# Performance work log

Hardware: AMD Instinct MI355X
Metric: run time of the kernel (lower is better)

The kernel has to match this reference:

```python
import jax, jax.numpy as jnp
import numpy as np

DIM = 1024
HEADS = 16
DIM_HEAD = 64


def setup_inputs() -> dict:
    key = jax.random.key(0)
    ks = jax.random.split(key, 6)
    b, n = 2, 2048
    x = jax.random.normal(ks[0], (b, n, DIM), dtype=jnp.float32)
    gamma = jnp.ones((DIM,), dtype=jnp.float32)
    w_qkv = jax.random.normal(ks[1], (DIM, 3 * HEADS * DIM_HEAD), dtype=jnp.float32) * (DIM ** -0.5)
    w_gates = jax.random.normal(ks[2], (DIM, HEADS), dtype=jnp.float32) * (DIM ** -0.5)
    b_gates = jnp.zeros((HEADS,), dtype=jnp.float32)
    w_out = jax.random.normal(ks[3], (HEADS * DIM_HEAD, DIM), dtype=jnp.float32) * ((HEADS * DIM_HEAD) ** -0.5)
    freqs = jax.random.uniform(ks[4], (DIM_HEAD // 2,), dtype=jnp.float32)
    return {"x": x, "gamma": gamma, "w_qkv": w_qkv, "w_gates": w_gates,
            "b_gates": b_gates, "w_out": w_out, "freqs": freqs}


def _rotate_half(t):
    # interleaved pairs: (x1, x2) -> (-x2, x1)
    tp = t.reshape(t.shape[:-1] + (t.shape[-1] // 2, 2))
    x1, x2 = tp[..., 0], tp[..., 1]
    return jnp.stack((-x2, x1), axis=-1).reshape(t.shape)


def reference(x, gamma, w_qkv, w_gates, b_gates, w_out, freqs):
    b, n, d = x.shape
    # RMSNorm variant: divide by L2 norm, scale by gamma * sqrt(dim)
    xn = x / jnp.linalg.norm(x, axis=-1, keepdims=True)
    xn = xn * gamma * (d ** 0.5)
    # QKV projection: (b, n, 3*H*D) -> q,k,v each (b, h, n, dh)
    qkv = xn @ w_qkv
    qkv = qkv.reshape(b, n, 3, HEADS, DIM_HEAD).transpose(2, 0, 3, 1, 4)
    q, k, v = qkv[0], qkv[1], qkv[2]
    # Inline RoPE (interleaved): freqs (n, dh)
    pos = jnp.arange(n, dtype=freqs.dtype)
    f = jnp.repeat(pos[:, None] * freqs[None, :], 2, axis=-1)  # (n, dh)
    cos_f, sin_f = jnp.cos(f), jnp.sin(f)
    q = q * cos_f + _rotate_half(q) * sin_f
    k = k * cos_f + _rotate_half(k) * sin_f
    # SDPA
    scale = DIM_HEAD ** -0.5
    scores = jnp.einsum('bhqd,bhkd->bhqk', q, k) * scale
    attn = jax.nn.softmax(scores, axis=-1)
    out = jnp.einsum('bhqk,bhkd->bhqd', attn, v)  # (b, h, n, dh)
    # per-head sigmoid gate from normalized input
    gates = xn @ w_gates + b_gates  # (b, n, h)
    out = out * jax.nn.sigmoid(gates.transpose(0, 2, 1))[..., None]
    # merge heads and output projection
    out = out.transpose(0, 2, 1, 3).reshape(b, n, HEADS * DIM_HEAD)
    return out @ w_out
```

## Files before the change

### kernel.cpp

```cpp
#include <hip/hip_runtime.h>

typedef __bf16 bf16_t;
typedef __bf16 bf16x8 __attribute__((ext_vector_type(8)));
typedef __bf16 bf16x4 __attribute__((ext_vector_type(4)));
typedef float f32x4 __attribute__((ext_vector_type(4)));

#define B_  2
#define N_  2048
#define D_  1024
#define H_  16
#define DH_ 64

#define GLL16(g, l) __builtin_amdgcn_global_load_lds( \
    (const __attribute__((address_space(1))) void*)(g), \
    (__attribute__((address_space(3))) void*)(l), 16, 0, 0)

__global__ __launch_bounds__(256) void k_rmsnorm_gates(const float* __restrict__ x,
    const float* __restrict__ gamma, const float* __restrict__ wg,
    const float* __restrict__ bg, bf16_t* __restrict__ xn, float* __restrict__ gsig) {
  int row = blockIdx.x;
  const float4* xr = (const float4*)(x + (size_t)row * D_);
  int tid = threadIdx.x;
  float4 v = xr[tid];
  float ss = v.x*v.x + v.y*v.y + v.z*v.z + v.w*v.w;
  #pragma unroll
  for (int off = 32; off > 0; off >>= 1) ss += __shfl_down(ss, off);
  __shared__ float red4[4];
  if ((tid & 63) == 0) red4[tid >> 6] = ss;
  __syncthreads();
  float scale = 32.0f * rsqrtf(red4[0] + red4[1] + red4[2] + red4[3]);
  float4 g = ((const float4*)gamma)[tid];
  bf16x4 o;
  o[0] = (bf16_t)(v.x * scale * g.x);
  o[1] = (bf16_t)(v.y * scale * g.y);
  o[2] = (bf16_t)(v.z * scale * g.z);
  o[3] = (bf16_t)(v.w * scale * g.w);
  *(bf16x4*)(xn + (size_t)row * D_ + tid * 4) = o;
  float xv[4] = {(float)o[0], (float)o[1], (float)o[2], (float)o[3]};
  float part[16];
  #pragma unroll
  for (int h = 0; h < 16; ++h) part[h] = 0.f;
  #pragma unroll
  for (int j = 0; j < 4; ++j) {
    const float4* wr = (const float4*)&wg[(size_t)(tid * 4 + j) * 16];
    #pragma unroll
    for (int q = 0; q < 4; ++q) {
      float4 w4 = wr[q];
      part[q * 4 + 0] += xv[j] * w4.x;
      part[q * 4 + 1] += xv[j] * w4.y;
      part[q * 4 + 2] += xv[j] * w4.z;
      part[q * 4 + 3] += xv[j] * w4.w;
    }
  }
  __shared__ float red[256][17];
  #pragma unroll
  for (int h = 0; h < 16; ++h) red[tid][h] = part[h];
  __syncthreads();
  int h = tid & 15, grp = tid >> 4;
  float s = 0.f;
  #pragma unroll
  for (int k = 0; k < 16; ++k) s += red[grp * 16 + k][h];
  __syncthreads();
  red[grp][h] = s;
  __syncthreads();
  if (tid < 16) {
    float acc = bg[tid];
    #pragma unroll
    for (int k = 0; k < 16; ++k) acc += red[k][tid];
    gsig[(size_t)row * 16 + tid] = 1.0f / (1.0f + __expf(-acc));
  }
}

__global__ __launch_bounds__(256) void k_transpose_cvt(const float* __restrict__ W,
    bf16_t* __restrict__ Wt, int R, int C) {
  __shared__ float tile[32][33];
  int c0 = blockIdx.x * 32, r0 = blockIdx.y * 32;
  int tx = threadIdx.x & 31, ty = threadIdx.x >> 5;
  #pragma unroll
  for (int i = 0; i < 4; ++i) {
    int r = ty + i * 8;
    tile[r][tx] = W[(size_t)(r0 + r) * C + c0 + tx];
  }
  __syncthreads();
  #pragma unroll
  for (int i = 0; i < 4; ++i) {
    int rr = ty + i * 8;
    Wt[(size_t)(c0 + rr) * R + r0 + tx] = (bf16_t)tile[tx][rr];
  }
}

template<bool OUT_BF16>
__global__ __launch_bounds__(256) void k_gemm_bt(const bf16_t* __restrict__ A,
    const bf16_t* __restrict__ Bt, void* __restrict__ Cp, int M, int N, int K) {
  constexpr int BK = 32;
  __shared__ __align__(16) bf16_t As[128 * BK];
  __shared__ __align__(16) bf16_t Bs[128 * BK];
  int tid = threadIdx.x, wave = tid >> 6, lane = tid & 63;
  int l16 = lane & 15, quad = lane >> 4;
  int bm = blockIdx.x * 128, bn = blockIdx.y * 128;
  int wm = (wave >> 1) * 64, wn = (wave & 1) * 64;
  int srow = wave * 32 + (lane >> 2);
  int scol = (lane & 3) * 8;
  const bf16_t* gA0 = &A [(size_t)(bm + srow)      * K + scol];
  const bf16_t* gA1 = &A [(size_t)(bm + srow + 16) * K + scol];
  const bf16_t* gB0 = &Bt[(size_t)(bn + srow)      * K + scol];
  const bf16_t* gB1 = &Bt[(size_t)(bn + srow + 16) * K + scol];
  bf16_t* lA0 = &As[(wave * 32)      * BK];
  bf16_t* lA1 = &As[(wave * 32 + 16) * BK];
  bf16_t* lB0 = &Bs[(wave * 32)      * BK];
  bf16_t* lB1 = &Bs[(wave * 32 + 16) * BK];
  f32x4 acc[4][4] = {};
  for (int k0 = 0; k0 < K; k0 += BK) {
    GLL16(gA0 + k0, lA0);
    GLL16(gA1 + k0, lA1);
    GLL16(gB0 + k0, lB0);
    GLL16(gB1 + k0, lB1);
    __syncthreads();
    bf16x8 af[4], bfr[4];
    #pragma unroll
    for (int t = 0; t < 4; ++t) {
      af[t]  = *(const bf16x8*)&As[(wm + t * 16 + l16) * BK + quad * 8];
      bfr[t] = *(const bf16x8*)&Bs[(wn + t * 16 + l16) * BK + quad * 8];
    }
    #pragma unroll
    for (int mt = 0; mt < 4; ++mt)
      #pragma unroll
      for (int nt = 0; nt < 4; ++nt)
        acc[mt][nt] = __builtin_amdgcn_mfma_f32_16x16x32_bf16(af[mt], bfr[nt], acc[mt][nt], 0, 0, 0);
    __syncthreads();
  }
  #pragma unroll
  for (int mt = 0; mt < 4; ++mt)
    #pragma unroll
    for (int nt = 0; nt < 4; ++nt)
      #pragma unroll
      for (int r = 0; r < 4; ++r) {
        int row = bm + wm + mt * 16 + quad * 4 + r;
        int col = bn + wn + nt * 16 + l16;
        float v = acc[mt][nt][r];
        if (OUT_BF16) ((bf16_t*)Cp)[(size_t)row * N + col] = (bf16_t)v;
        else          ((float*)Cp)[(size_t)row * N + col] = v;
      }
}

__global__ __launch_bounds__(256) void k_rope(const bf16_t* __restrict__ qkvb,
    const float* __restrict__ freqs, bf16_t* __restrict__ Qb, bf16_t* __restrict__ Kb) {
  int row = blockIdx.x, b = row >> 11, n = row & 2047;
  __shared__ float cs[32], sn[32];
  int tid = threadIdx.x;
  if (tid < 32) { float f = (float)n * freqs[tid]; cs[tid] = cosf(f); sn[tid] = sinf(f); }
  __syncthreads();
  const bf16_t* src = qkvb + (size_t)row * 3072;
  #pragma unroll
  for (int it = 0; it < 2; ++it) {
    int p = tid + 256 * it;
    int h = p >> 5, j = p & 31;
    size_t dst = ((size_t)(b * H_ + h) * N_ + n) * DH_ + 2 * j;
    float c = cs[j], s = sn[j];
    {
      float v0 = (float)src[h * 64 + 2 * j], v1 = (float)src[h * 64 + 2 * j + 1];
      union { bf16_t q[2]; unsigned u; } pk;
      pk.q[0] = (bf16_t)((v0 * c - v1 * s) * 0.125f);
      pk.q[1] = (bf16_t)((v1 * c + v0 * s) * 0.125f);
      *(unsigned*)&Qb[dst] = pk.u;
    }
    {
      float v0 = (float)src[1024 + h * 64 + 2 * j], v1 = (float)src[1024 + h * 64 + 2 * j + 1];
      union { bf16_t q[2]; unsigned u; } pk;
      pk.q[0] = (bf16_t)(v0 * c - v1 * s);
      pk.q[1] = (bf16_t)(v1 * c + v0 * s);
      *(unsigned*)&Kb[dst] = pk.u;
    }
  }
}

__global__ __launch_bounds__(256) void k_vtrans(const bf16_t* __restrict__ qkvb,
    bf16_t* __restrict__ Vb) {
  __shared__ bf16_t Vs[64][72];
  int bh = blockIdx.x, nt = blockIdx.y;
  int b = bh >> 4, h = bh & 15;
  int n0 = nt * 64;
  int tid = threadIdx.x;
  #pragma unroll
  for (int it = 0; it < 2; ++it) {
    int chunk = tid + 256 * it;
    int nl = chunk >> 3, c = (chunk & 7) * 8;
    *(bf16x8*)&Vs[nl][c] =
        *(const bf16x8*)&qkvb[(size_t)(b * N_ + n0 + nl) * 3072 + 2048 + h * 64 + c];
  }
  __syncthreads();
  #pragma unroll
  for (int it = 0; it < 2; ++it) {
    int chunk = tid + 256 * it;
    int d = chunk >> 3, nc = (chunk & 7) * 8;
    bf16x8 o;
    #pragma unroll
    for (int jj = 0; jj < 8; ++jj) o[jj] = Vs[nc + jj][d];
    *(bf16x8*)&Vb[((size_t)bh * DH_ + d) * N_ + n0 + nc] = o;
  }
}

__global__ __launch_bounds__(256) void k_flash(const bf16_t* __restrict__ Qb,
    const bf16_t* __restrict__ Kb, const bf16_t* __restrict__ Vb,
    const float* __restrict__ gsig, bf16_t* __restrict__ Ao) {
  __shared__ __align__(16) bf16_t Ks[2][64 * 72];
  __shared__ __align__(16) bf16_t Vt[2][64 * 72];
  __shared__ __align__(16) bf16_t Ps[4][32 * 72];
  int bh = blockIdx.y, b = bh >> 4, h = bh & 15;
  int tid = threadIdx.x, wave = tid >> 6, lane = tid & 63;
  int l16 = lane & 15, quad = lane >> 4;
  int qw = blockIdx.x * 128 + wave * 32;
  const bf16_t* Qh = Qb + (size_t)bh * N_ * DH_;
  const bf16_t* Kh = Kb + (size_t)bh * N_ * DH_;
  const bf16_t* Vh = Vb + (size_t)bh * DH_ * N_;
  bf16_t* Pw = Ps[wave];
  bf16x8 qf[2][2];
  #pragma unroll
  for (int qt = 0; qt < 2; ++qt)
    #pragma unroll
    for (int hf = 0; hf < 2; ++hf)
      qf[qt][hf] = *(const bf16x8*)&Qh[(size_t)(qw + qt * 16 + l16) * DH_ + hf * 32 + quad * 8];
  f32x4 accO[2][4] = {};
  float lsum[2] = {0.f, 0.f};
  int sk = tid >> 3;
  int sc = (tid & 7) * 8;
  bf16x8 rk0 = *(const bf16x8*)&Kh[(size_t)sk * DH_ + sc];
  bf16x8 rk1 = *(const bf16x8*)&Kh[(size_t)(sk + 32) * DH_ + sc];
  bf16x8 rv0 = *(const bf16x8*)&Vh[(size_t)sk * N_ + sc];
  bf16x8 rv1 = *(const bf16x8*)&Vh[(size_t)(sk + 32) * N_ + sc];
  *(bf16x8*)&Ks[0][sk * 72 + sc]        = rk0;
  *(bf16x8*)&Ks[0][(sk + 32) * 72 + sc] = rk1;
  *(bf16x8*)&Vt[0][sk * 72 + sc]        = rv0;
  *(bf16x8*)&Vt[0][(sk + 32) * 72 + sc] = rv1;
  __syncthreads();
  for (int k0 = 0; k0 < N_; k0 += 64) {
    int cur = (k0 >> 6) & 1;
    const bf16_t* Kc = Ks[cur];
    const bf16_t* Vc = Vt[cur];
    int kn = k0 + 64;
    if (kn < N_) {
      rk0 = *(const bf16x8*)&Kh[(size_t)(kn + sk) * DH_ + sc];
      rk1 = *(const bf16x8*)&Kh[(size_t)(kn + sk + 32) * DH_ + sc];
      rv0 = *(const bf16x8*)&Vh[(size_t)sk * N_ + kn + sc];
      rv1 = *(const bf16x8*)&Vh[(size_t)(sk + 32) * N_ + kn + sc];
    }
    f32x4 st[4][2];
    __builtin_amdgcn_s_setprio(1);
    #pragma unroll
    for (int kt = 0; kt < 4; ++kt) {
      bf16x8 kf0 = *(const bf16x8*)&Kc[(kt * 16 + l16) * 72 + quad * 8];
      bf16x8 kf1 = *(const bf16x8*)&Kc[(kt * 16 + l16) * 72 + 32 + quad * 8];
      #pragma unroll
      for (int qt = 0; qt < 2; ++qt) {
        f32x4 z = {};
        z = __builtin_amdgcn_mfma_f32_16x16x32_bf16(kf0, qf[qt][0], z, 0, 0, 0);
        z = __builtin_amdgcn_mfma_f32_16x16x32_bf16(kf1, qf[qt][1], z, 0, 0, 0);
        st[kt][qt] = z;
      }
    }
    __builtin_amdgcn_s_setprio(0);
    #pragma unroll
    for (int qt = 0; qt < 2; ++qt)
      #pragma unroll
      for (int kt = 0; kt < 4; ++kt) {
        bf16x4 pk;
        #pragma unroll
        for (int r = 0; r < 4; ++r) {
          float p = __expf(st[kt][qt][r] - 8.0f);
          lsum[qt] += p;
          pk[r] = (bf16_t)p;
        }
        *(bf16x4*)&Pw[(qt * 16 + l16) * 72 + kt * 16 + quad * 4] = pk;
      }
    bf16x8 pf[2][2];
    #pragma unroll
    for (int qt = 0; qt < 2; ++qt)
      #pragma unroll
      for (int hf = 0; hf < 2; ++hf)
        pf[qt][hf] = *(const bf16x8*)&Pw[(qt * 16 + l16) * 72 + hf * 32 + quad * 8];
    __builtin_amdgcn_s_setprio(1);
    #pragma unroll
    for (int dt = 0; dt < 4; ++dt)
      #pragma unroll
      for (int hf = 0; hf < 2; ++hf) {
        bf16x8 vf = *(const bf16x8*)&Vc[(dt * 16 + l16) * 72 + hf * 32 + quad * 8];
        #pragma unroll
        for (int qt = 0; qt < 2; ++qt)
          accO[qt][dt] = __builtin_amdgcn_mfma_f32_16x16x32_bf16(pf[qt][hf], vf, accO[qt][dt], 0, 0, 0);
      }
    __builtin_amdgcn_s_setprio(0);
    if (kn < N_) {
      int nb = cur ^ 1;
      *(bf16x8*)&Ks[nb][sk * 72 + sc]        = rk0;
      *(bf16x8*)&Ks[nb][(sk + 32) * 72 + sc] = rk1;
      *(bf16x8*)&Vt[nb][sk * 72 + sc]        = rv0;
      *(bf16x8*)&Vt[nb][(sk + 32) * 72 + sc] = rv1;
    }
    __syncthreads();
  }
  float lfull[2];
  #pragma unroll
  for (int qt = 0; qt < 2; ++qt) {
    float s = lsum[qt];
    s += __shfl_xor(s, 16);
    s += __shfl_xor(s, 32);
    lfull[qt] = s;
  }
  #pragma unroll
  for (int qt = 0; qt < 2; ++qt)
    #pragma unroll
    for (int r = 0; r < 4; ++r) {
      int qs = quad * 4 + r;
      float l_e = __shfl(lfull[qt], qs);
      int q = qw + qt * 16 + qs;
      float g = gsig[((size_t)b * N_ + q) * H_ + h];
      float ginv = g / l_e;
      #pragma unroll
      for (int dt = 0; dt < 4; ++dt)
        Ao[((size_t)b * N_ + q) * (H_ * DH_) + h * DH_ + dt * 16 + l16] =
            (bf16_t)(accO[qt][dt][r] * ginv);
    }
}

extern "C" void kernel_launch(void* const* d_in, const int* in_sizes, int n_in,
                              void* d_out, int out_size, void* d_ws, size_t ws_size,
                              hipStream_t stream) {
  (void)in_sizes; (void)n_in; (void)out_size; (void)ws_size;
  const float* x      = (const float*)d_in[0];
  const float* gamma  = (const float*)d_in[1];
  const float* w_qkv  = (const float*)d_in[2];
  const float* w_gate = (const float*)d_in[3];
  const float* b_gate = (const float*)d_in[4];
  const float* w_out  = (const float*)d_in[5];
  const float* freqs  = (const float*)d_in[6];
  float* out = (float*)d_out;
  char* ws = (char*)d_ws;
  bf16_t* xn    = (bf16_t*)(ws);
  bf16_t* wqkvT = (bf16_t*)(ws + ((size_t)8  << 20));
  bf16_t* woutT = (bf16_t*)(ws + ((size_t)14 << 20));
  bf16_t* Qb    = (bf16_t*)(ws + ((size_t)16 << 20));
  bf16_t* Kb    = (bf16_t*)(ws + ((size_t)24 << 20));
  bf16_t* Vb    = (bf16_t*)(ws + ((size_t)32 << 20));
  float*  gsig  = (float*) (ws + ((size_t)40 << 20));
  bf16_t* attn  = (bf16_t*)(ws + ((size_t)41 << 20));
  bf16_t* qkvb  = (bf16_t*)(ws + ((size_t)49 << 20));

  k_transpose_cvt<<<dim3(3072 / 32, 1024 / 32), 256, 0, stream>>>(w_qkv, wqkvT, 1024, 3072);
  k_transpose_cvt<<<dim3(1024 / 32, 1024 / 32), 256, 0, stream>>>(w_out, woutT, 1024, 1024);
  k_rmsnorm_gates<<<4096, 256, 0, stream>>>(x, gamma, w_gate, b_gate, xn, gsig);
  k_gemm_bt<true><<<dim3(32, 24), 256, 0, stream>>>(xn, wqkvT, (void*)qkvb, 4096, 3072, 1024);
  k_rope<<<4096, 256, 0, stream>>>(qkvb, freqs, Qb, Kb);
  k_vtrans<<<dim3(32, 32), 256, 0, stream>>>(qkvb, Vb);
  k_flash<<<dim3(16, 32), 256, 0, stream>>>(Qb, Kb, Vb, gsig, attn);
  k_gemm_bt<false><<<dim3(32, 8), 256, 0, stream>>>(attn, woutT, (void*)out, 4096, 1024, 1024);
}
```

Baseline: 252.6 us.

## Use exp2 softmax, MFMA row sums, XCD swizzle, vectorized RoPE, narrower out GEMM

Several unrelated changes land together. The flash kernel folds log2(e) into the Q scale and the fixed -8 offset into the accumulator init, so it can use exp2 directly. Row sums are now computed by MFMA against a vector of ones instead of scalar adds and shuffles. GEMM and flash blocks are remapped with an XCD-aware swizzle for better L2 locality, and RoPE now does one 16-byte vector load and store per thread. The output projection uses a 128x64 tile kernel, which doubles the block count for better occupancy at the cost of more A-tile reloads.

```diff
diff --git a/kernel.cpp b/kernel.cpp
--- a/kernel.cpp
+++ b/kernel.cpp
@@ -11,9 +11,24 @@
 #define H_  16
 #define DH_ 64
 
+#define QSCALE 0.18033688011112042f
+#define NEGC  -11.541560327111707f
+
+#if __has_builtin(__builtin_amdgcn_exp2f)
+#define EXP2F(x) __builtin_amdgcn_exp2f(x)
+#else
+#define EXP2F(x) exp2f(x)
+#endif
+
 #define GLL16(g, l) __builtin_amdgcn_global_load_lds( \
     (const __attribute__((address_space(1))) void*)(g), \
     (__attribute__((address_space(3))) void*)(l), 16, 0, 0)
+
+__device__ __forceinline__ int xcd_swizzle_id() {
+  int id = blockIdx.y * gridDim.x + blockIdx.x;
+  int cpx = (gridDim.x * gridDim.y) >> 3;
+  return (id & 7) * cpx + (id >> 3);
+}
 
 __global__ __launch_bounds__(256) void k_rmsnorm_gates(const float* __restrict__ x,
     const float* __restrict__ gamma, const float* __restrict__ wg,
@@ -97,7 +112,9 @@
   __shared__ __align__(16) bf16_t Bs[128 * BK];
   int tid = threadIdx.x, wave = tid >> 6, lane = tid & 63;
   int l16 = lane & 15, quad = lane >> 4;
-  int bm = blockIdx.x * 128, bn = blockIdx.y * 128;
+  int swz = xcd_swizzle_id();
+  int bxi = swz % gridDim.x, byi = swz / gridDim.x;
+  int bm = bxi * 128, bn = byi * 128;
   int wm = (wave >> 1) * 64, wn = (wave & 1) * 64;
   int srow = wave * 32 + (lane >> 2);
   int scol = (lane & 3) * 8;
@@ -143,6 +160,58 @@
       }
 }
 
+__global__ __launch_bounds__(256) void k_gemm_bt_n64(const bf16_t* __restrict__ A,
+    const bf16_t* __restrict__ Bt, float* __restrict__ C, int M, int N, int K) {
+  constexpr int BK = 32;
+  __shared__ __align__(16) bf16_t As[128 * BK];
+  __shared__ __align__(16) bf16_t Bs[64 * BK];
+  int tid = threadIdx.x, wave = tid >> 6, lane = tid & 63;
+  int l16 = lane & 15, quad = lane >> 4;
+  int swz = xcd_swizzle_id();
+  int bxi = swz % gridDim.x, byi = swz / gridDim.x;
+  int bm = bxi * 128, bn = byi * 64;
+  int wm = (wave >> 1) * 64, wn = (wave & 1) * 32;
+  int srow = wave * 32 + (lane >> 2);
+  int scol = (lane & 3) * 8;
+  const bf16_t* gA0 = &A [(size_t)(bm + srow)      * K + scol];
+  const bf16_t* gA1 = &A [(size_t)(bm + srow + 16) * K + scol];
+  int srB = wave * 16 + (lane >> 2);
+  const bf16_t* gB0 = &Bt[(size_t)(bn + srB) * K + scol];
+  bf16_t* lA0 = &As[(wave * 32)      * BK];
+  bf16_t* lA1 = &As[(wave * 32 + 16) * BK];
+  bf16_t* lB0 = &Bs[(wave * 16)      * BK];
+  f32x4 acc[4][2] = {};
+  for (int k0 = 0; k0 < K; k0 += BK) {
+    GLL16(gA0 + k0, lA0);
+    GLL16(gA1 + k0, lA1);
+    GLL16(gB0 + k0, lB0);
+    __syncthreads();
+    bf16x8 af[4], bfr[2];
+    #pragma unroll
+    for (int t = 0; t < 4; ++t)
+      af[t]  = *(const bf16x8*)&As[(wm + t * 16 + l16) * BK + quad * 8];
+    #pragma unroll
+    for (int t = 0; t < 2; ++t)
+      bfr[t] = *(const bf16x8*)&Bs[(wn + t * 16 + l16) * BK + quad * 8];
+    #pragma unroll
+    for (int mt = 0; mt < 4; ++mt)
+      #pragma unroll
+      for (int nt = 0; nt < 2; ++nt)
+        acc[mt][nt] = __builtin_amdgcn_mfma_f32_16x16x32_bf16(af[mt], bfr[nt], acc[mt][nt], 0, 0, 0);
+    __syncthreads();
+  }
+  #pragma unroll
+  for (int mt = 0; mt < 4; ++mt)
+    #pragma unroll
+    for (int nt = 0; nt < 2; ++nt)
+      #pragma unroll
+      for (int r = 0; r < 4; ++r) {
+        int row = bm + wm + mt * 16 + quad * 4 + r;
+        int col = bn + wn + nt * 16 + l16;
+        C[(size_t)row * N + col] = acc[mt][nt][r];
+      }
+}
+
 __global__ __launch_bounds__(256) void k_rope(const bf16_t* __restrict__ qkvb,
     const float* __restrict__ freqs, bf16_t* __restrict__ Qb, bf16_t* __restrict__ Kb) {
   int row = blockIdx.x, b = row >> 11, n = row & 2047;
@@ -151,27 +220,22 @@
   if (tid < 32) { float f = (float)n * freqs[tid]; cs[tid] = cosf(f); sn[tid] = sinf(f); }
   __syncthreads();
   const bf16_t* src = qkvb + (size_t)row * 3072;
-  #pragma unroll
-  for (int it = 0; it < 2; ++it) {
-    int p = tid + 256 * it;
-    int h = p >> 5, j = p & 31;
-    size_t dst = ((size_t)(b * H_ + h) * N_ + n) * DH_ + 2 * j;
-    float c = cs[j], s = sn[j];
-    {
-      float v0 = (float)src[h * 64 + 2 * j], v1 = (float)src[h * 64 + 2 * j + 1];
-      union { bf16_t q[2]; unsigned u; } pk;
-      pk.q[0] = (bf16_t)((v0 * c - v1 * s) * 0.125f);
-      pk.q[1] = (bf16_t)((v1 * c + v0 * s) * 0.125f);
-      *(unsigned*)&Qb[dst] = pk.u;
-    }
-    {
-      float v0 = (float)src[1024 + h * 64 + 2 * j], v1 = (float)src[1024 + h * 64 + 2 * j + 1];
-      union { bf16_t q[2]; unsigned u; } pk;
-      pk.q[0] = (bf16_t)(v0 * c - v1 * s);
-      pk.q[1] = (bf16_t)(v1 * c + v0 * s);
-      *(unsigned*)&Kb[dst] = pk.u;
-    }
-  }
+  int isK = tid >> 7;
+  int t = tid & 127;
+  int h = t >> 3, j8 = (t & 7) * 8;
+  bf16x8 v = *(const bf16x8*)&src[isK * 1024 + h * 64 + j8];
+  float qs = isK ? 1.0f : QSCALE;
+  bf16x8 o;
+  #pragma unroll
+  for (int i = 0; i < 4; ++i) {
+    int jj = (j8 >> 1) + i;
+    float c = cs[jj], s = sn[jj];
+    float v0 = (float)v[2 * i], v1 = (float)v[2 * i + 1];
+    o[2 * i]     = (bf16_t)((v0 * c - v1 * s) * qs);
+    o[2 * i + 1] = (bf16_t)((v1 * c + v0 * s) * qs);
+  }
+  bf16_t* dst = (isK ? Kb : Qb) + ((size_t)(b * H_ + h) * N_ + n) * DH_ + j8;
+  *(bf16x8*)dst = o;
 }
 
 __global__ __launch_bounds__(256) void k_vtrans(const bf16_t* __restrict__ qkvb,
@@ -206,10 +270,12 @@
   __shared__ __align__(16) bf16_t Ks[2][64 * 72];
   __shared__ __align__(16) bf16_t Vt[2][64 * 72];
   __shared__ __align__(16) bf16_t Ps[4][32 * 72];
-  int bh = blockIdx.y, b = bh >> 4, h = bh & 15;
+  int swz = xcd_swizzle_id();
+  int qblk = swz & 15, bh = swz >> 4;
+  int b = bh >> 4, h = bh & 15;
   int tid = threadIdx.x, wave = tid >> 6, lane = tid & 63;
   int l16 = lane & 15, quad = lane >> 4;
-  int qw = blockIdx.x * 128 + wave * 32;
+  int qw = qblk * 128 + wave * 32;
   const bf16_t* Qh = Qb + (size_t)bh * N_ * DH_;
   const bf16_t* Kh = Kb + (size_t)bh * N_ * DH_;
   const bf16_t* Vh = Vb + (size_t)bh * DH_ * N_;
@@ -220,8 +286,11 @@
     #pragma unroll
     for (int hf = 0; hf < 2; ++hf)
       qf[qt][hf] = *(const bf16x8*)&Qh[(size_t)(qw + qt * 16 + l16) * DH_ + hf * 32 + quad * 8];
+  bf16x8 onesf;
+  #pragma unroll
+  for (int i = 0; i < 8; ++i) onesf[i] = (bf16_t)1.0f;
   f32x4 accO[2][4] = {};
-  float lsum[2] = {0.f, 0.f};
+  f32x4 accL[2] = {};
   int sk = tid >> 3;
   int sc = (tid & 7) * 8;
   bf16x8 rk0 = *(const bf16x8*)&Kh[(size_t)sk * DH_ + sc];
@@ -233,6 +302,7 @@
   *(bf16x8*)&Vt[0][sk * 72 + sc]        = rv0;
   *(bf16x8*)&Vt[0][(sk + 32) * 72 + sc] = rv1;
   __syncthreads();
+  const f32x4 zinit = {NEGC, NEGC, NEGC, NEGC};
   for (int k0 = 0; k0 < N_; k0 += 64) {
     int cur = (k0 >> 6) & 1;
     const bf16_t* Kc = Ks[cur];
@@ -252,7 +322,7 @@
       bf16x8 kf1 = *(const bf16x8*)&Kc[(kt * 16 + l16) * 72 + 32 + quad * 8];
       #pragma unroll
       for (int qt = 0; qt < 2; ++qt) {
-        f32x4 z = {};
+        f32x4 z = zinit;
         z = __builtin_amdgcn_mfma_f32_16x16x32_bf16(kf0, qf[qt][0], z, 0, 0, 0);
         z = __builtin_amdgcn_mfma_f32_16x16x32_bf16(kf1, qf[qt][1], z, 0, 0, 0);
         st[kt][qt] = z;
@@ -265,11 +335,8 @@
       for (int kt = 0; kt < 4; ++kt) {
         bf16x4 pk;
         #pragma unroll
-        for (int r = 0; r < 4; ++r) {
-          float p = __expf(st[kt][qt][r] - 8.0f);
-          lsum[qt] += p;
-          pk[r] = (bf16_t)p;
-        }
+        for (int r = 0; r < 4; ++r)
+          pk[r] = (bf16_t)EXP2F(st[kt][qt][r]);
         *(bf16x4*)&Pw[(qt * 16 + l16) * 72 + kt * 16 + quad * 4] = pk;
       }
     bf16x8 pf[2][2];
@@ -279,6 +346,11 @@
       for (int hf = 0; hf < 2; ++hf)
         pf[qt][hf] = *(const bf16x8*)&Pw[(qt * 16 + l16) * 72 + hf * 32 + quad * 8];
     __builtin_amdgcn_s_setprio(1);
+    #pragma unroll
+    for (int qt = 0; qt < 2; ++qt) {
+      accL[qt] = __builtin_amdgcn_mfma_f32_16x16x32_bf16(pf[qt][0], onesf, accL[qt], 0, 0, 0);
+      accL[qt] = __builtin_amdgcn_mfma_f32_16x16x32_bf16(pf[qt][1], onesf, accL[qt], 0, 0, 0);
+    }
     #pragma unroll
     for (int dt = 0; dt < 4; ++dt)
       #pragma unroll
@@ -298,23 +370,13 @@
     }
     __syncthreads();
   }
-  float lfull[2];
-  #pragma unroll
-  for (int qt = 0; qt < 2; ++qt) {
-    float s = lsum[qt];
-    s += __shfl_xor(s, 16);
-    s += __shfl_xor(s, 32);
-    lfull[qt] = s;
-  }
   #pragma unroll
   for (int qt = 0; qt < 2; ++qt)
     #pragma unroll
     for (int r = 0; r < 4; ++r) {
-      int qs = quad * 4 + r;
-      float l_e = __shfl(lfull[qt], qs);
-      int q = qw + qt * 16 + qs;
+      int q = qw + qt * 16 + quad * 4 + r;
       float g = gsig[((size_t)b * N_ + q) * H_ + h];
-      float ginv = g / l_e;
+      float ginv = g / accL[qt][r];
       #pragma unroll
       for (int dt = 0; dt < 4; ++dt)
         Ao[((size_t)b * N_ + q) * (H_ * DH_) + h * DH_ + dt * 16 + l16] =
@@ -352,5 +414,5 @@
   k_rope<<<4096, 256, 0, stream>>>(qkvb, freqs, Qb, Kb);
   k_vtrans<<<dim3(32, 32), 256, 0, stream>>>(qkvb, Vb);
   k_flash<<<dim3(16, 32), 256, 0, stream>>>(Qb, Kb, Vb, gsig, attn);
-  k_gemm_bt<false><<<dim3(32, 8), 256, 0, stream>>>(attn, woutT, (void*)out, 4096, 1024, 1024);
-}
+  k_gemm_bt_n64<<<dim3(32, 16), 256, 0, stream>>>(attn, woutT, out, 4096, 1024, 1024);
+}
```

Measured after the change: 239.2 us. 1.06x faster.
